# Kernel optimization log

Measured on AMD Instinct MI355X. Metric: run time of the kernel, lower is better.

The kernel has to match this reference:

```python
import jax, jax.numpy as jnp
import numpy as np
from jax import lax

VOCAB = 32000
WORD_DIM = 300
CHANNEL = 400
ATTN_DIM = 200
KSIZE = 3
B, N_WORD = 32768, 30


def setup_inputs() -> dict:
    key = jax.random.key(0)
    ks = jax.random.split(key, 7)
    encoded_title = jax.random.randint(ks[0], (B, N_WORD), 0, VOCAB)
    emb = jax.random.normal(ks[1], (VOCAB, WORD_DIM), dtype=jnp.float32)
    emb = emb.at[0].set(0.0)  # padding_idx=0
    # Conv1d weight [out, in, k] (torch layout), xavier-ish scale
    conv_w = jax.random.normal(ks[2], (CHANNEL, WORD_DIM, KSIZE), dtype=jnp.float32) * 0.05
    conv_b = jnp.zeros((CHANNEL,), dtype=jnp.float32)
    v = jax.random.normal(ks[3], (CHANNEL, ATTN_DIM), dtype=jnp.float32) * 0.07
    vb = jnp.zeros((ATTN_DIM,), dtype=jnp.float32)
    q = jax.random.normal(ks[4], (ATTN_DIM, 1), dtype=jnp.float32) * 0.1
    return {"encoded_title": encoded_title, "emb": emb, "conv_w": conv_w,
            "conv_b": conv_b, "v": v, "vb": vb, "q": q}


def reference(encoded_title, emb, conv_w, conv_b, v, vb, q):
    # Embedding lookup: [B, N, word_dim]  (dropout is identity in eval mode)
    W = emb[encoded_title]
    # Conv1d over the word axis, padding='SAME' (torch padding=1, k=3).
    # torch weight [out, in, k] -> WIO kernel [k, in, out]
    kernel = jnp.transpose(conv_w, (2, 1, 0))
    C = lax.conv_general_dilated(
        W, kernel, window_strides=(1,), padding="SAME",
        dimension_numbers=("NWC", "WIO", "NWC")) + conv_b  # [B, N, channel]
    # Additive attention scores: tanh(C @ v + vb) @ q -> [B, N]
    a = jnp.squeeze(jnp.tanh(C @ v + vb) @ q, -1)
    # Faithful to the original: Softmax(dim=0) normalizes over the BATCH axis.
    alpha = jax.nn.softmax(a, axis=0)
    # Batched weighted pooling (replaces per-sample python loop)
    e = jnp.einsum("bn,bnc->bc", alpha, C)  # [B, channel]
    return e
```

## Files before the change

### kernel.cpp

```cpp
#include <hip/hip_runtime.h>
#include <cstdint>
#include <cstddef>

#define BT     32768
#define NW     30
#define VOCAB  32000
#define WD     300
#define CH     400
#define AD     200

#define EMB_LD   320
#define E3_LDB   640
#define U_LD     928
#define WCT_ROWS 512
#define EXPA_LD  32

#define TWO_LOG2E 2.8853900817779268f
#define QRANGE 14.0f
#define QSC  (127.0f / QRANGE)
#define QDEC (QRANGE / 127.0f)

typedef __attribute__((ext_vector_type(8))) short bf16x8;
typedef __attribute__((ext_vector_type(4))) float f32x4;

__device__ __forceinline__ float blo(unsigned int u) {
  union { unsigned int i; float f; } x; x.i = u << 16; return x.f;
}
__device__ __forceinline__ float bhi(unsigned int u) {
  union { unsigned int i; float f; } x; x.i = u & 0xffff0000u; return x.f;
}
__device__ __forceinline__ unsigned short f2bf(float f) {
  union { float f; unsigned int i; } x; x.f = f;
  unsigned int r = x.i + 0x7FFFu + ((x.i >> 16) & 1u);
  return (unsigned short)(r >> 16);
}
__device__ __forceinline__ unsigned int pack2bf(float a, float b) {
  return (unsigned int)f2bf(a) | ((unsigned int)f2bf(b) << 16);
}
__device__ __forceinline__ float fexp2(float x) {
#if __has_builtin(__builtin_amdgcn_exp2f)
  return __builtin_amdgcn_exp2f(x);
#else
  float r; asm volatile("v_exp_f32 %0, %1" : "=v"(r) : "v"(x)); return r;
#endif
}
#define SB(u, j) ((int)(signed char)(((u) >> (8 * (j))) & 0xffu))

__global__ void prep_MtT_bias(const float* __restrict__ conv_w,
                              const float* __restrict__ conv_b,
                              const float* __restrict__ v,
                              const float* __restrict__ vb,
                              const float* __restrict__ q,
                              unsigned short* __restrict__ MtT,
                              float* __restrict__ bias2,
                              float* __restrict__ q2s,
                              float* __restrict__ qsum) {
  int blk = blockIdx.x;
  int i = threadIdx.x;
  if (blk < 640) {
    float val = 0.f;
    if (blk < 600 && i < WD) {
      int k = blk / AD, d = blk - k * AD;
      float acc = 0.f;
      #pragma unroll 4
      for (int c = 0; c < CH; ++c)
        acc += conv_w[(c * WD + i) * 3 + k] * v[c * AD + d];
      val = TWO_LOG2E * acc;
    }
    MtT[blk * EMB_LD + i] = f2bf(val);
  } else if (blk == 640) {
    if (i < AD) {
      float acc = vb[i];
      #pragma unroll 4
      for (int c = 0; c < CH; ++c)
        acc += conv_b[c] * v[c * AD + i];
      bias2[i] = TWO_LOG2E * acc;
    }
  } else {
    if (i < AD) q2s[i] = -2.0f * q[i];
    if (i == 0) {
      float s = 0.f;
      for (int j = 0; j < AD; ++j) s += q[j];
      qsum[0] = s;
    }
  }
}

__global__ void prep_WcT(const float* __restrict__ conv_w, unsigned short* __restrict__ WcT) {
  int c = blockIdx.x;
  for (int kk = threadIdx.x; kk < U_LD; kk += 256) {
    float val = 0.f;
    if (c < CH && kk < 900) {
      int k = kk / WD, i = kk - k * WD;
      val = conv_w[(c * WD + i) * 3 + k];
    }
    WcT[(size_t)c * U_LD + kk] = f2bf(val);
  }
}

__global__ void prep_emb_bf16(const float* __restrict__ emb, unsigned short* __restrict__ embb) {
  int idx = blockIdx.x * 256 + threadIdx.x;
  if (idx >= VOCAB * EMB_LD) return;
  int r = idx / EMB_LD, c = idx - r * EMB_LD;
  embb[idx] = (c < WD) ? f2bf(emb[(size_t)r * WD + c]) : (unsigned short)0;
}

template<int MODE>
__global__ __launch_bounds__(256) void gemm_mfma(
    const unsigned short* __restrict__ A, int lda,
    const unsigned short* __restrict__ Bt, int ldb,
    void* __restrict__ Cp, int ldc, int N, int K,
    const float* __restrict__ bias_m, const float* __restrict__ bias_n,
    const float* __restrict__ e3bias) {
  __shared__ unsigned short As[128][40];
  __shared__ unsigned short Bs[128][40];
  int tid = threadIdx.x;
  int lane = tid & 63, wave = tid >> 6;

  int gx = gridDim.x;
  int nwg = gx * (int)gridDim.y;
  int orig = blockIdx.y * gx + blockIdx.x;
  int xcd = orig & 7, qq = nwg >> 3, rr = nwg & 7;
  int wg = (xcd < rr ? xcd * (qq + 1) : rr * (qq + 1) + (xcd - rr) * qq) + (orig >> 3);
  int row0 = (wg / gx) * 128, col0 = (wg % gx) * 128;

  int wm = (wave & 1) * 64, wn = (wave >> 1) * 64;
  int lr = lane & 15, quad = lane >> 4;

  f32x4 acc[4][4];
  #pragma unroll
  for (int i = 0; i < 4; ++i)
    #pragma unroll
    for (int j = 0; j < 4; ++j) acc[i][j] = (f32x4){0.f, 0.f, 0.f, 0.f};

  int r0 = tid >> 2, ko0 = (tid & 3) * 8;
  int r1 = (tid + 256) >> 2, ko1 = ((tid + 256) & 3) * 8;

  for (int k0 = 0; k0 < K; k0 += 32) {
    float4 av0 = *(const float4*)(A + (size_t)(row0 + r0) * lda + k0 + ko0);
    float4 av1 = *(const float4*)(A + (size_t)(row0 + r1) * lda + k0 + ko1);
    float4 bv0 = *(const float4*)(Bt + (size_t)(col0 + r0) * ldb + k0 + ko0);
    float4 bv1 = *(const float4*)(Bt + (size_t)(col0 + r1) * ldb + k0 + ko1);
    __syncthreads();
    *(float4*)&As[r0][ko0] = av0;
    *(float4*)&As[r1][ko1] = av1;
    *(float4*)&Bs[r0][ko0] = bv0;
    *(float4*)&Bs[r1][ko1] = bv1;
    __syncthreads();

    bf16x8 af[4], bfr[4];
    #pragma unroll
    for (int mi = 0; mi < 4; ++mi)
      af[mi] = *(const bf16x8*)&As[wm + mi * 16 + lr][quad * 8];
    #pragma unroll
    for (int ni = 0; ni < 4; ++ni)
      bfr[ni] = *(const bf16x8*)&Bs[wn + ni * 16 + lr][quad * 8];
    #pragma unroll
    for (int mi = 0; mi < 4; ++mi)
      #pragma unroll
      for (int ni = 0; ni < 4; ++ni)
        acc[mi][ni] = __builtin_amdgcn_mfma_f32_16x16x32_bf16(
            af[mi], bfr[ni], acc[mi][ni], 0, 0, 0);
  }

  if (MODE == 1) {
    signed char* C = (signed char*)Cp;
    #pragma unroll
    for (int mi = 0; mi < 4; ++mi)
      #pragma unroll
      for (int ni = 0; ni < 4; ++ni) {
        int c = col0 + wn + ni * 16 + lr;
        float cb = (e3bias && c >= 200 && c < 400) ? e3bias[c - 200] : 0.f;
        #pragma unroll
        for (int reg = 0; reg < 4; ++reg) {
          int r = row0 + wm + mi * 16 + quad * 4 + reg;
          float x = (acc[mi][ni][reg] + cb) * QSC;
          int qi = (int)rintf(x);
          qi = qi > 127 ? 127 : (qi < -127 ? -127 : qi);
          C[(size_t)r * ldc + c] = (signed char)qi;
        }
      }
  } else {
    float* C = (float*)Cp;
    #pragma unroll
    for (int mi = 0; mi < 4; ++mi)
      #pragma unroll
      for (int ni = 0; ni < 4; ++ni) {
        int c = col0 + wn + ni * 16 + lr;
        if (c < N) {
          float bn = bias_n[c];
          #pragma unroll
          for (int reg = 0; reg < 4; ++reg) {
            int r = row0 + wm + mi * 16 + quad * 4 + reg;
            C[(size_t)r * ldc + c] = acc[mi][ni][reg] + bias_m[r] * bn;
          }
        }
      }
  }
}

__global__ __launch_bounds__(256) void scores_kernel(
    const int* __restrict__ tok, const signed char* __restrict__ E3,
    const float* __restrict__ q2s, const float* __restrict__ qsum,
    float* __restrict__ expa) {
  __shared__ float qs[AD];
  int tid = threadIdx.x;
  if (tid < AD) qs[tid] = q2s[tid];
  __syncthreads();
  int wave = tid >> 6, lane = tid & 63;
  int b = blockIdx.x * 4 + wave;
  int tk = tok[b * NW + ((lane < NW) ? lane : 0)];
  int d0 = (lane < 50) ? lane * 4 : 0;
  float4 qv = make_float4(0.f, 0.f, 0.f, 0.f);
  if (lane < 50) qv = *(const float4*)&qs[d0];
  float Qsum = qsum[0];
  float myscore = 0.f;

  int t0r = __shfl(tk, 0, 64);
  const signed char* r0p = E3 + (size_t)(unsigned)t0r * E3_LDB + d0;
  unsigned int a0 = *(const unsigned int*)(r0p);
  unsigned int a1 = *(const unsigned int*)(r0p + 200);
  unsigned int a2 = *(const unsigned int*)(r0p + 400);

  int P0 = 0, P1 = 0, P2 = 0, P3 = 0;
  int Q0 = 0, Q1 = 0, Q2 = 0, Q3 = 0;

  #pragma unroll
  for (int m = 0; m < NW; ++m) {
    unsigned int u0 = a0, u1 = a1, u2 = a2;
    if (m + 1 < NW) {
      int tn = __shfl(tk, m + 1, 64);
      const signed char* rp = E3 + (size_t)(unsigned)tn * E3_LDB + d0;
      a0 = *(const unsigned int*)(rp);
      a1 = *(const unsigned int*)(rp + 200);
      a2 = *(const unsigned int*)(rp + 400);
    }
    if (m > 0) {
      float s0 = QDEC * (float)(P0 + SB(u2, 0));
      float s1 = QDEC * (float)(P1 + SB(u2, 1));
      float s2 = QDEC * (float)(P2 + SB(u2, 2));
      float s3 = QDEC * (float)(P3 + SB(u2, 3));
      float acc;
      acc = qv.x * __builtin_amdgcn_rcpf(fexp2(s0) + 1.0f);
      acc = fmaf(qv.y, __builtin_amdgcn_rcpf(fexp2(s1) + 1.0f), acc);
      acc = fmaf(qv.z, __builtin_amdgcn_rcpf(fexp2(s2) + 1.0f), acc);
      acc = fmaf(qv.w, __builtin_amdgcn_rcpf(fexp2(s3) + 1.0f), acc);
      #pragma unroll
      for (int off = 1; off < 64; off <<= 1) acc += __shfl_xor(acc, off, 64);
      myscore = (lane == m - 1) ? acc : myscore;
    }
    P0 = Q0 + SB(u1, 0); P1 = Q1 + SB(u1, 1);
    P2 = Q2 + SB(u1, 2); P3 = Q3 + SB(u1, 3);
    Q0 = SB(u0, 0); Q1 = SB(u0, 1);
    Q2 = SB(u0, 2); Q3 = SB(u0, 3);
  }
  {
    float s0 = QDEC * (float)P0, s1 = QDEC * (float)P1;
    float s2 = QDEC * (float)P2, s3 = QDEC * (float)P3;
    float acc;
    acc = qv.x * __builtin_amdgcn_rcpf(fexp2(s0) + 1.0f);
    acc = fmaf(qv.y, __builtin_amdgcn_rcpf(fexp2(s1) + 1.0f), acc);
    acc = fmaf(qv.z, __builtin_amdgcn_rcpf(fexp2(s2) + 1.0f), acc);
    acc = fmaf(qv.w, __builtin_amdgcn_rcpf(fexp2(s3) + 1.0f), acc);
    #pragma unroll
    for (int off = 1; off < 64; off <<= 1) acc += __shfl_xor(acc, off, 64);
    myscore = (lane == NW - 1) ? acc : myscore;
  }
  float e = __expf(Qsum + myscore);
  if (lane < NW) expa[(size_t)b * EXPA_LD + lane] = e;
}

__global__ __launch_bounds__(256) void softmax_part(const float* __restrict__ expa,
                                                    float* __restrict__ part) {
  __shared__ float P[256][33];
  int tid = threadIdx.x;
  const float* row = expa + (size_t)(blockIdx.x * 256 + tid) * EXPA_LD;
  #pragma unroll
  for (int j = 0; j < 7; ++j) {
    float4 vv = *(const float4*)(row + j * 4);
    P[tid][j * 4] = vv.x; P[tid][j * 4 + 1] = vv.y;
    P[tid][j * 4 + 2] = vv.z; P[tid][j * 4 + 3] = vv.w;
  }
  P[tid][28] = row[28]; P[tid][29] = row[29];
  __syncthreads();
  int wave = tid >> 6, lane = tid & 63;
  for (int n = wave * 8; n < wave * 8 + 8 && n < NW; ++n) {
    float s = P[lane * 4][n] + P[lane * 4 + 1][n] + P[lane * 4 + 2][n] + P[lane * 4 + 3][n];
    #pragma unroll
    for (int off = 32; off > 0; off >>= 1) s += __shfl_down(s, off, 64);
    if (lane == 0) part[n * 128 + blockIdx.x] = s;
  }
}

__global__ void softmax_fin(const float* __restrict__ part, float* __restrict__ rinv) {
  int n = blockIdx.x;
  int lane = threadIdx.x;
  float s = part[n * 128 + lane] + part[n * 128 + 64 + lane];
  #pragma unroll
  for (int off = 32; off > 0; off >>= 1) s += __shfl_down(s, off, 64);
  if (lane == 0) rinv[n] = 1.0f / s;
}

__global__ __launch_bounds__(192) void build_U(
    const int* __restrict__ tok, const unsigned short* __restrict__ embb,
    const float* __restrict__ expa, const float* __restrict__ rinv,
    unsigned short* __restrict__ U, float* __restrict__ Salpha) {
  int b = blockIdx.x;
  int tid = threadIdx.x;
  __shared__ float alpha[NW];
  __shared__ int ltok[NW];
  if (tid < NW) {
    ltok[tid] = tok[b * NW + tid];
    alpha[tid] = expa[(size_t)b * EXPA_LD + tid] * rinv[tid];
  }
  __syncthreads();
  if (tid == 0) {
    float s = 0.f;
    #pragma unroll
    for (int n = 0; n < NW; ++n) s += alpha[n];
    Salpha[b] = s;
  }
  unsigned short* Ub = U + (size_t)b * U_LD;
  if (tid < 150) {
    float a0 = 0.f, a1 = 0.f, a2 = 0.f;
    float b0 = 0.f, b1 = 0.f, b2 = 0.f;
    #pragma unroll 2
    for (int m = 0; m < NW; ++m) {
      int t = ltok[m];
      float w0 = (m + 1 < NW) ? alpha[m + 1] : 0.f;
      float w1 = alpha[m];
      float w2 = (m >= 1) ? alpha[m - 1] : 0.f;
      unsigned int u = *(const unsigned int*)(embb + (size_t)t * EMB_LD + 2 * tid);
      float x = blo(u), y = bhi(u);
      a0 = fmaf(w0, x, a0); b0 = fmaf(w0, y, b0);
      a1 = fmaf(w1, x, a1); b1 = fmaf(w1, y, b1);
      a2 = fmaf(w2, x, a2); b2 = fmaf(w2, y, b2);
    }
    *(unsigned int*)(Ub + 2 * tid)       = pack2bf(a0, b0);
    *(unsigned int*)(Ub + 300 + 2 * tid) = pack2bf(a1, b1);
    *(unsigned int*)(Ub + 600 + 2 * tid) = pack2bf(a2, b2);
  } else if (tid < 164) {
    *(unsigned int*)(Ub + 900 + 2 * (tid - 150)) = 0u;
  }
}

extern "C" void kernel_launch(void* const* d_in, const int* in_sizes, int n_in,
                              void* d_out, int out_size, void* d_ws, size_t ws_size,
                              hipStream_t stream) {
  const int*   tok    = (const int*)d_in[0];
  const float* emb    = (const float*)d_in[1];
  const float* conv_w = (const float*)d_in[2];
  const float* conv_b = (const float*)d_in[3];
  const float* v      = (const float*)d_in[4];
  const float* vb     = (const float*)d_in[5];
  const float* q      = (const float*)d_in[6];
  float* out = (float*)d_out;

  char* wb = (char*)d_ws;
  float* bias2           = (float*)(wb + 0);
  float* rinv            = (float*)(wb + 4096);
  float* part            = (float*)(wb + 8192);
  float* q2s             = (float*)(wb + 23552);
  float* qsum            = (float*)(wb + 24448);
  float* Salpha          = (float*)(wb + 24576);
  float* expa            = (float*)(wb + 155648);
  unsigned short* embb   = (unsigned short*)(wb + 5070848);
  unsigned short* MtT    = (unsigned short*)(wb + 25550848);
  unsigned short* WcT    = (unsigned short*)(wb + 25960448);
  unsigned short* big    = (unsigned short*)(wb + 26910720);
  signed char* E3 = (signed char*)big;
  unsigned short* U = big;

  hipLaunchKernelGGL(prep_MtT_bias, dim3(642), dim3(320), 0, stream,
                     conv_w, conv_b, v, vb, q, MtT, bias2, q2s, qsum);
  hipLaunchKernelGGL(prep_WcT, dim3(WCT_ROWS), dim3(256), 0, stream, conv_w, WcT);
  hipLaunchKernelGGL(prep_emb_bf16, dim3((VOCAB * EMB_LD) / 256), dim3(256), 0, stream,
                     emb, embb);
  hipLaunchKernelGGL((gemm_mfma<1>), dim3(E3_LDB / 128, VOCAB / 128), dim3(256), 0, stream,
                     embb, EMB_LD, MtT, EMB_LD, (void*)E3, E3_LDB, E3_LDB, EMB_LD,
                     (const float*)nullptr, (const float*)nullptr, bias2);
  hipLaunchKernelGGL(scores_kernel, dim3(BT / 4), dim3(256), 0, stream,
                     tok, E3, q2s, qsum, expa);
  hipLaunchKernelGGL(softmax_part, dim3(128), dim3(256), 0, stream, expa, part);
  hipLaunchKernelGGL(softmax_fin, dim3(NW), dim3(64), 0, stream, part, rinv);
  hipLaunchKernelGGL(build_U, dim3(BT), dim3(192), 0, stream,
                     tok, embb, expa, rinv, U, Salpha);
  hipLaunchKernelGGL((gemm_mfma<0>), dim3(WCT_ROWS / 128, BT / 128), dim3(256), 0, stream,
                     U, U_LD, WcT, U_LD, (void*)out, CH, CH, U_LD,
                     Salpha, conv_b, (const float*)nullptr);
}
```

Baseline: 438.9 us.

## Use offset-uint8 E3 with float decode, paired sigmoid rcp, LDS score reduction

Stores the quantized E3 table as uint8 with a +128 offset so the scores kernel decodes bytes directly to float, folding the offset into a constant bias. Adjacent sigmoid terms are combined over a shared denominator, which halves the reciprocal count. The per-word 64-lane shuffle butterfly is replaced by one xor shuffle plus a shared-memory transpose and a vectorized sum after a block barrier. This cuts ALU and cross-lane shuffle work per word, at the cost of LDS traffic and a __syncthreads.

Result: faster. 420.2 us (-4.3%).

```diff
diff --git a/kernel.cpp b/kernel.cpp
--- a/kernel.cpp
+++ b/kernel.cpp
@@ -19,6 +19,7 @@
 #define QRANGE 14.0f
 #define QSC  (127.0f / QRANGE)
 #define QDEC (QRANGE / 127.0f)
+#define QB3  (-384.0f * QDEC)
 
 typedef __attribute__((ext_vector_type(8))) short bf16x8;
 typedef __attribute__((ext_vector_type(4))) float f32x4;
@@ -44,7 +45,7 @@
   float r; asm volatile("v_exp_f32 %0, %1" : "=v"(r) : "v"(x)); return r;
 #endif
 }
-#define SB(u, j) ((int)(signed char)(((u) >> (8 * (j))) & 0xffu))
+#define UBF(u, j) ((float)(((u) >> (8 * (j))) & 0xffu))
 
 __global__ void prep_MtT_bias(const float* __restrict__ conv_w,
                               const float* __restrict__ conv_b,
@@ -164,7 +165,7 @@
   }
 
   if (MODE == 1) {
-    signed char* C = (signed char*)Cp;
+    unsigned char* C = (unsigned char*)Cp;
     #pragma unroll
     for (int mi = 0; mi < 4; ++mi)
       #pragma unroll
@@ -177,7 +178,7 @@
           float x = (acc[mi][ni][reg] + cb) * QSC;
           int qi = (int)rintf(x);
           qi = qi > 127 ? 127 : (qi < -127 ? -127 : qi);
-          C[(size_t)r * ldc + c] = (signed char)qi;
+          C[(size_t)r * ldc + c] = (unsigned char)(qi + 128);
         }
       }
   } else {
@@ -200,10 +201,11 @@
 }
 
 __global__ __launch_bounds__(256) void scores_kernel(
-    const int* __restrict__ tok, const signed char* __restrict__ E3,
+    const int* __restrict__ tok, const unsigned char* __restrict__ E3,
     const float* __restrict__ q2s, const float* __restrict__ qsum,
     float* __restrict__ expa) {
   __shared__ float qs[AD];
+  __shared__ __align__(16) float red[4][NW][36];
   int tid = threadIdx.x;
   if (tid < AD) qs[tid] = q2s[tid];
   __syncthreads();
@@ -213,60 +215,75 @@
   int d0 = (lane < 50) ? lane * 4 : 0;
   float4 qv = make_float4(0.f, 0.f, 0.f, 0.f);
   if (lane < 50) qv = *(const float4*)&qs[d0];
+  float s01 = qv.x + qv.y, s23 = qv.z + qv.w;
   float Qsum = qsum[0];
-  float myscore = 0.f;
+  float* myred = &red[wave][0][lane >> 1];
 
   int t0r = __shfl(tk, 0, 64);
-  const signed char* r0p = E3 + (size_t)(unsigned)t0r * E3_LDB + d0;
+  const unsigned char* r0p = E3 + (size_t)(unsigned)t0r * E3_LDB + d0;
   unsigned int a0 = *(const unsigned int*)(r0p);
   unsigned int a1 = *(const unsigned int*)(r0p + 200);
   unsigned int a2 = *(const unsigned int*)(r0p + 400);
 
-  int P0 = 0, P1 = 0, P2 = 0, P3 = 0;
-  int Q0 = 0, Q1 = 0, Q2 = 0, Q3 = 0;
+  float P0 = 0.f, P1 = 0.f, P2 = 0.f, P3 = 0.f;
+  float Q0 = 128.f, Q1 = 128.f, Q2 = 128.f, Q3 = 128.f;
 
   #pragma unroll
   for (int m = 0; m < NW; ++m) {
     unsigned int u0 = a0, u1 = a1, u2 = a2;
     if (m + 1 < NW) {
       int tn = __shfl(tk, m + 1, 64);
-      const signed char* rp = E3 + (size_t)(unsigned)tn * E3_LDB + d0;
+      const unsigned char* rp = E3 + (size_t)(unsigned)tn * E3_LDB + d0;
       a0 = *(const unsigned int*)(rp);
       a1 = *(const unsigned int*)(rp + 200);
       a2 = *(const unsigned int*)(rp + 400);
     }
     if (m > 0) {
-      float s0 = QDEC * (float)(P0 + SB(u2, 0));
-      float s1 = QDEC * (float)(P1 + SB(u2, 1));
-      float s2 = QDEC * (float)(P2 + SB(u2, 2));
-      float s3 = QDEC * (float)(P3 + SB(u2, 3));
-      float acc;
-      acc = qv.x * __builtin_amdgcn_rcpf(fexp2(s0) + 1.0f);
-      acc = fmaf(qv.y, __builtin_amdgcn_rcpf(fexp2(s1) + 1.0f), acc);
-      acc = fmaf(qv.z, __builtin_amdgcn_rcpf(fexp2(s2) + 1.0f), acc);
-      acc = fmaf(qv.w, __builtin_amdgcn_rcpf(fexp2(s3) + 1.0f), acc);
-      #pragma unroll
-      for (int off = 1; off < 64; off <<= 1) acc += __shfl_xor(acc, off, 64);
-      myscore = (lane == m - 1) ? acc : myscore;
-    }
-    P0 = Q0 + SB(u1, 0); P1 = Q1 + SB(u1, 1);
-    P2 = Q2 + SB(u1, 2); P3 = Q3 + SB(u1, 3);
-    Q0 = SB(u0, 0); Q1 = SB(u0, 1);
-    Q2 = SB(u0, 2); Q3 = SB(u0, 3);
+      float e0 = fexp2(fmaf(P0 + UBF(u2, 0), QDEC, QB3));
+      float e1 = fexp2(fmaf(P1 + UBF(u2, 1), QDEC, QB3));
+      float e2 = fexp2(fmaf(P2 + UBF(u2, 2), QDEC, QB3));
+      float e3 = fexp2(fmaf(P3 + UBF(u2, 3), QDEC, QB3));
+      float n01 = fmaf(qv.x, e1, s01); n01 = fmaf(qv.y, e0, n01);
+      float n23 = fmaf(qv.z, e3, s23); n23 = fmaf(qv.w, e2, n23);
+      float d01 = fmaf(e0, e1, (e0 + e1) + 1.0f);
+      float d23 = fmaf(e2, e3, (e2 + e3) + 1.0f);
+      float acc = n01 * __builtin_amdgcn_rcpf(d01);
+      acc = fmaf(n23, __builtin_amdgcn_rcpf(d23), acc);
+      acc += __shfl_xor(acc, 1, 64);
+      myred[(m - 1) * 36] = acc;
+    }
+    P0 = Q0 + UBF(u1, 0); P1 = Q1 + UBF(u1, 1);
+    P2 = Q2 + UBF(u1, 2); P3 = Q3 + UBF(u1, 3);
+    Q0 = UBF(u0, 0); Q1 = UBF(u0, 1);
+    Q2 = UBF(u0, 2); Q3 = UBF(u0, 3);
   }
   {
-    float s0 = QDEC * (float)P0, s1 = QDEC * (float)P1;
-    float s2 = QDEC * (float)P2, s3 = QDEC * (float)P3;
-    float acc;
-    acc = qv.x * __builtin_amdgcn_rcpf(fexp2(s0) + 1.0f);
-    acc = fmaf(qv.y, __builtin_amdgcn_rcpf(fexp2(s1) + 1.0f), acc);
-    acc = fmaf(qv.z, __builtin_amdgcn_rcpf(fexp2(s2) + 1.0f), acc);
-    acc = fmaf(qv.w, __builtin_amdgcn_rcpf(fexp2(s3) + 1.0f), acc);
-    #pragma unroll
-    for (int off = 1; off < 64; off <<= 1) acc += __shfl_xor(acc, off, 64);
-    myscore = (lane == NW - 1) ? acc : myscore;
-  }
-  float e = __expf(Qsum + myscore);
+    float e0 = fexp2(fmaf(P0 + 128.f, QDEC, QB3));
+    float e1 = fexp2(fmaf(P1 + 128.f, QDEC, QB3));
+    float e2 = fexp2(fmaf(P2 + 128.f, QDEC, QB3));
+    float e3 = fexp2(fmaf(P3 + 128.f, QDEC, QB3));
+    float n01 = fmaf(qv.x, e1, s01); n01 = fmaf(qv.y, e0, n01);
+    float n23 = fmaf(qv.z, e3, s23); n23 = fmaf(qv.w, e2, n23);
+    float d01 = fmaf(e0, e1, (e0 + e1) + 1.0f);
+    float d23 = fmaf(e2, e3, (e2 + e3) + 1.0f);
+    float acc = n01 * __builtin_amdgcn_rcpf(d01);
+    acc = fmaf(n23, __builtin_amdgcn_rcpf(d23), acc);
+    acc += __shfl_xor(acc, 1, 64);
+    myred[(NW - 1) * 36] = acc;
+  }
+  __syncthreads();
+  int n = lane & 31; if (n >= NW) n = 0;
+  int half = lane >> 5;
+  const float4* rp4 = (const float4*)&red[wave][n][half * 16];
+  float4 s4 = rp4[0];
+  #pragma unroll
+  for (int j = 1; j < 4; ++j) {
+    float4 vv = rp4[j];
+    s4.x += vv.x; s4.y += vv.y; s4.z += vv.z; s4.w += vv.w;
+  }
+  float tot = (s4.x + s4.y) + (s4.z + s4.w);
+  tot += __shfl_xor(tot, 32, 64);
+  float e = __expf(Qsum + tot);
   if (lane < NW) expa[(size_t)b * EXPA_LD + lane] = e;
 }
 
@@ -368,7 +385,7 @@
   unsigned short* MtT    = (unsigned short*)(wb + 25550848);
   unsigned short* WcT    = (unsigned short*)(wb + 25960448);
   unsigned short* big    = (unsigned short*)(wb + 26910720);
-  signed char* E3 = (signed char*)big;
+  unsigned char* E3 = (unsigned char*)big;
   unsigned short* U = big;
 
   hipLaunchKernelGGL(prep_MtT_bias, dim3(642), dim3(320), 0, stream,
```
